# Kernel optimization log

Measured on AMD Instinct MI355X. Metric: run time of the kernel, lower is better.

## Reference

```python
import jax, jax.numpy as jnp
import numpy as np

TOP_K = 2


def setup_inputs() -> dict:
    key = jax.random.key(0)
    k0, k1, k2, k3, k4 = jax.random.split(key, 5)
    B, S, H, I, E = 4, 2048, 1024, 2816, 8
    s_h = 1.0 / np.sqrt(H)
    s_i = 1.0 / np.sqrt(I)
    return {
        "x": jax.random.normal(k0, (B, S, H), jnp.float32),
        # nn.Linear weights are stored as [out_features, in_features]
        "w_router": jax.random.normal(k1, (E, H), jnp.float32) * s_h,   # gate: H -> E
        "w_gate": jax.random.normal(k2, (E, I, H), jnp.float32) * s_h,  # per-expert gate_proj
        "w_up": jax.random.normal(k3, (E, I, H), jnp.float32) * s_h,    # per-expert up_proj
        "w_down": jax.random.normal(k4, (E, H, I), jnp.float32) * s_i,  # per-expert down_proj
    }


def reference(x, w_router, w_gate, w_up, w_down):
    B, S, H = x.shape
    E = w_router.shape[0]
    xf = x.reshape(-1, H)                      # [T, H], T = B*S

    # --- Router: softmax over experts, top-k, renormalize weights ---
    logits = jnp.einsum("th,eh->te", xf, w_router)        # [T, E]
    probs = jax.nn.softmax(logits, axis=-1)
    topw, topi = jax.lax.top_k(probs, TOP_K)              # [T, k]
    topw = topw / jnp.sum(topw, axis=-1, keepdims=True)

    # Per-token combine weight for each expert: sum_k w[t,k] * 1[idx[t,k]==e]
    onehot = (topi[..., None] == jnp.arange(E)).astype(x.dtype)  # [T, k, E]
    combine = jnp.einsum("tk,tke->te", topw, onehot)             # [T, E]

    # --- Experts: SwiGLU MLP per expert on all tokens, masked combine ---
    # (masked-dense in the original == gather-compute mathematically,
    # since silu(0)*0 = 0 and the projections have no bias)
    gate = jax.nn.silu(jnp.einsum("th,eih->eti", xf, w_gate))    # [E, T, I]
    up = jnp.einsum("th,eih->eti", xf, w_up)                     # [E, T, I]
    down = jnp.einsum("eti,ehi->eth", gate * up, w_down)         # [E, T, H]

    out = jnp.einsum("eth,te->th", down, combine)                # [T, H]
    return out.reshape(B, S, H)
```

## Files before the change

### kernel.cpp

```cpp
#include <hip/hip_runtime.h>

#define TT 8192
#define HD 1024
#define ID 2816
#define NE 8
#define NID2 (2*ID)

typedef __attribute__((ext_vector_type(8))) short short8;
typedef __attribute__((ext_vector_type(4))) float f32x4;

#define WS_TOP2I 0
#define WS_TOP2W 65536
#define WS_CNT   131072
#define WS_OFF   131136
#define WS_CUR   131200
#define WS_TMAP  131328
#define WS_SLOTW 196864
#define WS_T2S   262400
#define WS_XB    1048576ULL
#define WS_WGU   (WS_XB  + 16777216ULL)
#define WS_WDB   (WS_WGU + 92274688ULL)
#define WS_ACT   (WS_WDB + 46137344ULL)

__device__ __forceinline__ unsigned int pack_bf2(float lo, float hi) {
  unsigned int ul = __builtin_bit_cast(unsigned int, lo) + 0x8000u;
  unsigned int uh = __builtin_bit_cast(unsigned int, hi) + 0x8000u;
  return (uh & 0xffff0000u) | (ul >> 16);
}

__device__ __forceinline__ unsigned short f2bf(float f) {
  unsigned int u = __builtin_bit_cast(unsigned int, f);
  return (unsigned short)((u + 0x8000u) >> 16);
}

__device__ __forceinline__ void gload16(const void* g, void* l) {
  __builtin_amdgcn_global_load_lds(
      (const __attribute__((address_space(1))) unsigned int*)g,
      (__attribute__((address_space(3))) unsigned int*)l, 16, 0, 0);
}

__global__ __launch_bounds__(256) void router_kernel(
    const float* __restrict__ x, const float* __restrict__ wr,
    int* __restrict__ top2i, float* __restrict__ top2w,
    unsigned short* __restrict__ xb)
{
  int tid  = threadIdx.x;
  int lane = tid & 63;
  int t    = blockIdx.x * 4 + (tid >> 6);

  const float4* xp = (const float4*)(x + (size_t)t * HD + lane * 16);
  float4 xv[4];
  #pragma unroll
  for (int j = 0; j < 4; ++j) xv[j] = xp[j];

  uint4 v0, v1;
  v0.x = pack_bf2(xv[0].x, xv[0].y); v0.y = pack_bf2(xv[0].z, xv[0].w);
  v0.z = pack_bf2(xv[1].x, xv[1].y); v0.w = pack_bf2(xv[1].z, xv[1].w);
  v1.x = pack_bf2(xv[2].x, xv[2].y); v1.y = pack_bf2(xv[2].z, xv[2].w);
  v1.z = pack_bf2(xv[3].x, xv[3].y); v1.w = pack_bf2(xv[3].z, xv[3].w);
  uint4* xrow = (uint4*)(xb + (size_t)t * HD + lane * 16);
  xrow[0] = v0; xrow[1] = v1;

  float acc[NE];
  #pragma unroll
  for (int e = 0; e < NE; ++e) {
    const float4* wp = (const float4*)(wr + (size_t)e * HD + lane * 16);
    float s = 0.f;
    #pragma unroll
    for (int j = 0; j < 4; ++j) {
      float4 w = wp[j];
      s += xv[j].x * w.x + xv[j].y * w.y + xv[j].z * w.z + xv[j].w * w.w;
    }
    acc[e] = s;
  }
  #pragma unroll
  for (int d = 1; d < 64; d <<= 1) {
    #pragma unroll
    for (int e = 0; e < NE; ++e) acc[e] += __shfl_xor(acc[e], d, 64);
  }
  int   i0 = 0; float m0 = acc[0];
  #pragma unroll
  for (int e = 1; e < NE; ++e) if (acc[e] > m0) { m0 = acc[e]; i0 = e; }
  int   i1 = -1; float m1 = -3.4e38f;
  #pragma unroll
  for (int e = 0; e < NE; ++e) if (e != i0 && acc[e] > m1) { m1 = acc[e]; i1 = e; }

  float e1 = __expf(m1 - m0);
  float w0 = 1.f / (1.f + e1);
  float w1 = e1 * w0;

  if (lane == 0) {
    top2i[2 * t] = i0;  top2i[2 * t + 1] = i1;
    top2w[2 * t] = w0;  top2w[2 * t + 1] = w1;
  }
}

__global__ __launch_bounds__(256) void count_scan_kernel(
    const int* __restrict__ top2i,
    int* __restrict__ counts, int* __restrict__ offsets, int* __restrict__ cursors)
{
  __shared__ int s_cnt[NE];
  int tid = threadIdx.x;
  if (tid < NE) s_cnt[tid] = 0;
  __syncthreads();

  int c0=0,c1=0,c2=0,c3=0,c4=0,c5=0,c6=0,c7=0;
  for (int t = tid; t < TT; t += 256) {
    int e0 = top2i[2 * t], e1 = top2i[2 * t + 1];
    c0 += __popcll(__ballot(e0 == 0)) + __popcll(__ballot(e1 == 0));
    c1 += __popcll(__ballot(e0 == 1)) + __popcll(__ballot(e1 == 1));
    c2 += __popcll(__ballot(e0 == 2)) + __popcll(__ballot(e1 == 2));
    c3 += __popcll(__ballot(e0 == 3)) + __popcll(__ballot(e1 == 3));
    c4 += __popcll(__ballot(e0 == 4)) + __popcll(__ballot(e1 == 4));
    c5 += __popcll(__ballot(e0 == 5)) + __popcll(__ballot(e1 == 5));
    c6 += __popcll(__ballot(e0 == 6)) + __popcll(__ballot(e1 == 6));
    c7 += __popcll(__ballot(e0 == 7)) + __popcll(__ballot(e1 == 7));
  }
  if ((tid & 63) == 0) {
    atomicAdd(&s_cnt[0], c0); atomicAdd(&s_cnt[1], c1);
    atomicAdd(&s_cnt[2], c2); atomicAdd(&s_cnt[3], c3);
    atomicAdd(&s_cnt[4], c4); atomicAdd(&s_cnt[5], c5);
    atomicAdd(&s_cnt[6], c6); atomicAdd(&s_cnt[7], c7);
  }
  __syncthreads();
  if (tid == 0) {
    int run = 0;
    #pragma unroll
    for (int e = 0; e < NE; ++e) {
      counts[e] = s_cnt[e]; offsets[e] = run; cursors[e] = run; run += s_cnt[e];
    }
    offsets[NE] = run;
  }
}

__global__ __launch_bounds__(256) void place_kernel(
    const int* __restrict__ top2i, const float* __restrict__ top2w,
    int* __restrict__ cursors,
    int* __restrict__ token_map, float* __restrict__ slot_w, int* __restrict__ tok2slot)
{
  int tid  = threadIdx.x;
  int lane = tid & 63;
  int t    = blockIdx.x * 256 + tid;

  #pragma unroll
  for (int k = 0; k < 2; ++k) {
    int   e = top2i[2 * t + k];
    float w = top2w[2 * t + k];
    #pragma unroll
    for (int ee = 0; ee < NE; ++ee) {
      unsigned long long m = __ballot(e == ee);
      if (e == ee) {
        int leader = __ffsll((long long)m) - 1;
        int pre    = __popcll(m & ((1ull << lane) - 1ull));
        int base   = 0;
        if (lane == leader) base = atomicAdd(&cursors[ee], (int)__popcll(m));
        base = __shfl(base, leader, 64);
        token_map[base + pre] = t;
        slot_w[base + pre]    = w;
        tok2slot[2 * t + k]   = base + pre;
      }
    }
  }
}

__global__ __launch_bounds__(256) void cvt_wgu_kernel(
    const float* __restrict__ wg, const float* __restrict__ wu,
    unsigned short* __restrict__ wgu)
{
  int e   = blockIdx.y;
  int idx = blockIdx.x * 256 + threadIdx.x;
  int col8 = idx & 127;
  int rr   = idx >> 7;
  int blk  = rr >> 8;
  int win  = rr & 255;
  const float* srow = (win < 128)
      ? wg + ((size_t)e * ID + blk * 128 + win) * HD
      : wu + ((size_t)e * ID + blk * 128 + (win - 128)) * HD;
  const float4* p = (const float4*)(srow + col8 * 8);
  float4 a = p[0], b = p[1];
  uint4 v;
  v.x = pack_bf2(a.x, a.y); v.y = pack_bf2(a.z, a.w);
  v.z = pack_bf2(b.x, b.y); v.w = pack_bf2(b.z, b.w);
  *(uint4*)(wgu + ((size_t)e * NID2 + rr) * HD + col8 * 8) = v;
}

__global__ __launch_bounds__(256) void cvt_bf16_kernel(
    const float* __restrict__ in, unsigned short* __restrict__ out, int n8)
{
  int i = blockIdx.x * 256 + threadIdx.x;
  if (i >= n8) return;
  const float4* p = (const float4*)(in + (size_t)i * 8);
  float4 a = p[0], b = p[1];
  uint4 v;
  v.x = pack_bf2(a.x, a.y); v.y = pack_bf2(a.z, a.w);
  v.z = pack_bf2(b.x, b.y); v.w = pack_bf2(b.z, b.w);
  ((uint4*)out)[i] = v;
}


#define VW2() asm volatile("s_waitcnt vmcnt(2)" ::: "memory")
#define VW0() asm volatile("s_waitcnt vmcnt(0)" ::: "memory")
#define LG0() asm volatile("s_waitcnt lgkmcnt(0)" ::: "memory")
#define BAR() __builtin_amdgcn_s_barrier()

#define DBUF(u) (ldsc + (((u) & 1) ? 65536u : 0u) + (unsigned)tid * 16)
#define ISS_B01(u) { size_t k1 = (size_t)((u) * 64); char* db = DBUF(u); \
    gload16(bS[0] + k1, db + 32768); gload16(bS[1] + k1, db + 40960); }
#define ISS_B23(u) { size_t k1 = (size_t)((u) * 64); char* db = DBUF(u); \
    gload16(bS[2] + k1, db + 49152); gload16(bS[3] + k1, db + 57344); }
#define ISS_A02(u) { size_t k1 = (size_t)((u) * 64); char* db = DBUF(u); \
    gload16(aS[0] + k1, db);         gload16(aS[2] + k1, db + 16384); }
#define ISS_A13(u) { size_t k1 = (size_t)((u) * 64); char* db = DBUF(u); \
    gload16(aS[1] + k1, db + 8192);  gload16(aS[3] + k1, db + 24576); }

#define RD_B(KB) \
    _Pragma("unroll") for (int n = 0; n < 4; ++n) \
      bfr[n] = *(const short8*)(sB + (wc * 64 + n * 16 + arow) * 128 + ((KB) ^ rxor));
#define RD_A(MH, KB) \
    _Pragma("unroll") for (int m = 0; m < 4; ++m) \
      af[m] = *(const short8*)(sa + (wr * 128 + (MH) * 64 + m * 16 + arow) * 128 + ((KB) ^ rxor));
#define MF(MB) \
    __builtin_amdgcn_s_setprio(1); \
    _Pragma("unroll") for (int m = 0; m < 4; ++m) \
      _Pragma("unroll") for (int n = 0; n < 4; ++n) \
        acc[(MB) + m][n] = __builtin_amdgcn_mfma_f32_16x16x32_bf16(af[m], bfr[n], acc[(MB) + m][n], 0, 0, 0); \
    __builtin_amdgcn_s_setprio(0);

#define KTILE(t, NT) { \
    const char* sa = ldsc + (((t) & 1) ? 65536u : 0u); \
    const char* sB = sa + 32768; \
    short8 bfr[4], af[4]; \
    int u1 = (t) + 1, u2 = (t) + 2; \
     RD_B(kq) RD_A(0, kq) \
    if (u1 < (NT)) ISS_B23(u1); \
    BAR(); LG0(); MF(0) BAR(); \
     RD_A(1, kq) \
    if (u1 < (NT)) ISS_A02(u1); \
    BAR(); LG0(); MF(4) BAR(); \
     RD_B(64 + kq) RD_A(0, 64 + kq) \
    if (u1 < (NT)) ISS_A13(u1); \
    BAR(); LG0(); MF(0) BAR(); \
     RD_A(1, 64 + kq) \
    if (u2 < (NT)) { ISS_B01(u2); VW2(); } \
    else if (u1 < (NT)) { VW0(); } \
    BAR(); LG0(); MF(4) BAR(); }

#define KLOOP(NT) { \
    ISS_B01(0); ISS_B23(0); ISS_A02(0); ISS_A13(0); \
    ISS_B01(1); \
    VW2(); BAR(); \
    for (int t = 0; t < (NT); ++t) KTILE(t, (NT)); }

#define XCD_DECODE(NX, NY) \
  int nwg  = (NX) * (NY) * NE; \
  int flat = blockIdx.x + (NX) * (blockIdx.y + (NY) * blockIdx.z); \
  int qq   = nwg >> 3; \
  int wg   = (flat & 7) * qq + (flat >> 3); \
  int bx   = wg % (NX); \
  int rem  = wg / (NX); \
  int y    = rem % (NY); \
  int e    = rem / (NY);

__global__ __launch_bounds__(512) void gemm1_fast(
    const unsigned short* __restrict__ xb, const unsigned short* __restrict__ wgu,
    const int* __restrict__ counts, const int* __restrict__ offsets,
    const int* __restrict__ token_map, unsigned short* __restrict__ act)
{
  extern __shared__ char smem[];
  char* ldsc = smem;

  XCD_DECODE(8, 22)
  int cnt = counts[e];
  int off = offsets[e];

  int tid  = threadIdx.x;
  int lane = tid & 63;
  int w    = tid >> 6;
  int wr   = w >> 2;
  int wc   = w & 3;

  int srow0 = tid >> 3;
  int colE  = (((tid & 7) ^ ((tid >> 3) & 7)) << 3);
  int rxor  = (lane & 7) << 4;
  int arow  = lane & 15;
  int kq    = (lane >> 4) << 4;
  int prow  = (lane >> 4) << 2;

  for (int t0 = bx * 256; t0 < cnt; t0 += 2048) {
    const unsigned short* aS[4];
    const unsigned short* bS[4];
    #pragma unroll
    for (int j = 0; j < 4; ++j) {
      int row  = srow0 + 64 * j;
      int tr   = t0 + row;
      int slot = off + (tr < cnt ? tr : cnt - 1);
      aS[j] = xb  + (size_t)token_map[slot] * HD + colE;
      bS[j] = wgu + ((size_t)e * NID2 + (size_t)y * 256 + row) * HD + colE;
    }

    f32x4 zf = {0.f, 0.f, 0.f, 0.f};
    f32x4 acc[8][4];
    #pragma unroll
    for (int m = 0; m < 8; ++m)
      #pragma unroll
      for (int n = 0; n < 4; ++n) acc[m][n] = zf;

    KLOOP(HD / 64);

    __syncthreads();
    float* xch = (float*)smem;
    if (wc >= 2) {
      float* base = xch + (size_t)((wr * 2 + (wc - 2)) * 8192);
      #pragma unroll
      for (int m = 0; m < 8; ++m)
        #pragma unroll
        for (int n = 0; n < 4; ++n)
          #pragma unroll
          for (int r = 0; r < 4; ++r)
            base[(m * 16 + prow + r) * 64 + n * 16 + arow] = acc[m][n][r];
    }
    __syncthreads();
    if (wc < 2) {
      const float* base = xch + (size_t)((wr * 2 + wc) * 8192);
      int i0 = y * 128 + wc * 64;
      #pragma unroll
      for (int m = 0; m < 8; ++m) {
        #pragma unroll
        for (int r = 0; r < 4; ++r) {
          int row = wr * 128 + m * 16 + prow + r;
          int tr2 = t0 + row;
          if (tr2 >= cnt) continue;
          size_t ob = (size_t)(off + tr2) * ID + i0 + arow;
          #pragma unroll
          for (int n = 0; n < 4; ++n) {
            float g = acc[m][n][r];
            float u = base[(m * 16 + prow + r) * 64 + n * 16 + arow];
            float h = g * u / (1.f + __expf(-g));
            act[ob + n * 16] = f2bf(h);
          }
        }
      }
    }
    __syncthreads();
  }
}

__global__ __launch_bounds__(512) void gemm2_fast(
    const unsigned short* __restrict__ act, const unsigned short* __restrict__ wdb,
    const int* __restrict__ counts, const int* __restrict__ offsets,
    float* __restrict__ down)
{
  extern __shared__ char smem[];
  char* ldsc = smem;

  XCD_DECODE(8, 4)
  int cnt = counts[e];
  int off = offsets[e];

  int tid  = threadIdx.x;
  int lane = tid & 63;
  int w    = tid >> 6;
  int wr   = w >> 2;
  int wc   = w & 3;

  int srow0 = tid >> 3;
  int colE  = (((tid & 7) ^ ((tid >> 3) & 7)) << 3);
  int rxor  = (lane & 7) << 4;
  int arow  = lane & 15;
  int kq    = (lane >> 4) << 4;
  int prow  = (lane >> 4) << 2;

  for (int t0 = bx * 256; t0 < cnt; t0 += 2048) {
    const unsigned short* aS[4];
    const unsigned short* bS[4];
    #pragma unroll
    for (int j = 0; j < 4; ++j) {
      int row  = srow0 + 64 * j;
      int tr   = t0 + row;
      int slot = off + (tr < cnt ? tr : cnt - 1);
      aS[j] = act + (size_t)slot * ID + colE;
      bS[j] = wdb + ((size_t)e * HD + (size_t)y * 256 + row) * ID + colE;
    }

    f32x4 zf = {0.f, 0.f, 0.f, 0.f};
    f32x4 acc[8][4];
    #pragma unroll
    for (int m = 0; m < 8; ++m)
      #pragma unroll
      for (int n = 0; n < 4; ++n) acc[m][n] = zf;

    KLOOP(ID / 64);

    #pragma unroll
    for (int m = 0; m < 8; ++m) {
      #pragma unroll
      for (int r = 0; r < 4; ++r) {
        int row = wr * 128 + m * 16 + prow + r;
        int tr2 = t0 + row;
        if (tr2 >= cnt) continue;
        float* ob = down + (size_t)(off + tr2) * HD + (size_t)y * 256 + wc * 64 + arow;
        #pragma unroll
        for (int n = 0; n < 4; ++n)
          ob[n * 16] = acc[m][n][r];
      }
    }
    __syncthreads();
  }
}

__global__ __launch_bounds__(256) void combine_kernel(
    const float* __restrict__ down, const float* __restrict__ slot_w,
    const int* __restrict__ tok2slot, float* __restrict__ out)
{
  int t   = blockIdx.x;
  int tid = threadIdx.x;
  int s0  = tok2slot[2 * t], s1 = tok2slot[2 * t + 1];
  float w0 = slot_w[s0], w1 = slot_w[s1];
  const float4* d0 = (const float4*)(down + (size_t)s0 * HD) + tid;
  const float4* d1 = (const float4*)(down + (size_t)s1 * HD) + tid;
  float4 a = *d0, b = *d1;
  float4 o;
  o.x = w0 * a.x + w1 * b.x;  o.y = w0 * a.y + w1 * b.y;
  o.z = w0 * a.z + w1 * b.z;  o.w = w0 * a.w + w1 * b.w;
  ((float4*)(out + (size_t)t * HD))[tid] = o;
}

extern "C" void kernel_launch(void* const* d_in, const int* in_sizes, int n_in,
                              void* d_out, int out_size, void* d_ws, size_t ws_size,
                              hipStream_t stream) {
  const float* x        = (const float*)d_in[0];
  const float* w_router = (const float*)d_in[1];
  const float* w_gate   = (const float*)d_in[2];
  const float* w_up     = (const float*)d_in[3];
  const float* w_down   = (const float*)d_in[4];

  char* ws = (char*)d_ws;
  int*   top2i    = (int*)(ws + WS_TOP2I);
  float* top2w    = (float*)(ws + WS_TOP2W);
  int*   counts   = (int*)(ws + WS_CNT);
  int*   offsets  = (int*)(ws + WS_OFF);
  int*   cursors  = (int*)(ws + WS_CUR);
  int*   tmap     = (int*)(ws + WS_TMAP);
  float* slotw    = (float*)(ws + WS_SLOTW);
  int*   tok2slot = (int*)(ws + WS_T2S);
  unsigned short* xb  = (unsigned short*)(ws + WS_XB);
  unsigned short* wgu = (unsigned short*)(ws + WS_WGU);
  unsigned short* wdb = (unsigned short*)(ws + WS_WDB);
  unsigned short* act = (unsigned short*)(ws + WS_ACT);
  float*          down = (float*)(ws + WS_WGU);

  hipFuncSetAttribute((const void*)gemm1_fast,
                      hipFuncAttributeMaxDynamicSharedMemorySize, 131072);
  hipFuncSetAttribute((const void*)gemm2_fast,
                      hipFuncAttributeMaxDynamicSharedMemorySize, 131072);

  router_kernel<<<TT / 4, 256, 0, stream>>>(x, w_router, top2i, top2w, xb);
  count_scan_kernel<<<1, 256, 0, stream>>>(top2i, counts, offsets, cursors);
  place_kernel<<<TT / 256, 256, 0, stream>>>(top2i, top2w, cursors, tmap, slotw, tok2slot);
  cvt_wgu_kernel<<<dim3(2816, NE), 256, 0, stream>>>(w_gate, w_up, wgu);
  cvt_bf16_kernel<<<11264, 256, 0, stream>>>(w_down, wdb, NE * HD * ID / 8);

  gemm1_fast<<<dim3(8, 22, NE), 512, 131072, stream>>>(xb, wgu, counts, offsets, tmap, act);
  gemm2_fast<<<dim3(8, 4, NE), 512, 131072, stream>>>(act, wdb, counts, offsets, down);
  combine_kernel<<<TT, 256, 0, stream>>>(down, slotw, tok2slot, (float*)d_out);
}
```

Baseline: 594.1 us.

## Restructure GEMM K-loop pipeline with fewer barriers and inline-asm LDS reads

Rewrites the K-tile loop of the expert GEMM. Per-tile barriers drop from eight to two: each tile now waits on vmcnt(1), syncs once, and then issues the next tile's global-to-LDS loads in between the LDS reads and MFMA groups. The last tile is peeled so the main loop has no branches. LDS fragment reads now go through explicit ds_read_b128 inline asm with a sched_barrier after lgkmcnt waits, to control how instructions are ordered. The cost is a shorter prefetch distance, since the B01 half is no longer issued two tiles ahead, so global-load latency may be less well hidden.

```diff
diff --git a/kernel.cpp b/kernel.cpp
--- a/kernel.cpp
+++ b/kernel.cpp
@@ -37,6 +37,13 @@
   __builtin_amdgcn_global_load_lds(
       (const __attribute__((address_space(1))) unsigned int*)g,
       (__attribute__((address_space(3))) unsigned int*)l, 16, 0, 0);
+}
+
+__device__ __forceinline__ short8 dsr(const void* p) {
+  short8 d;
+  unsigned a = (unsigned)(size_t)(__attribute__((address_space(3))) const char*)p;
+  asm volatile("ds_read_b128 %0, %1" : "=v"(d) : "v"(a));
+  return d;
 }
 
 __global__ __launch_bounds__(256) void router_kernel(
@@ -198,9 +205,10 @@
 }
 
 
-#define VW2() asm volatile("s_waitcnt vmcnt(2)" ::: "memory")
+#define VW1() asm volatile("s_waitcnt vmcnt(1)" ::: "memory")
 #define VW0() asm volatile("s_waitcnt vmcnt(0)" ::: "memory")
-#define LG0() asm volatile("s_waitcnt lgkmcnt(0)" ::: "memory")
+#define LGS() { asm volatile("s_waitcnt lgkmcnt(0)" ::: "memory"); \
+                __builtin_amdgcn_sched_barrier(0); }
 #define BAR() __builtin_amdgcn_s_barrier()
 
 #define DBUF(u) (ldsc + (((u) & 1) ? 65536u : 0u) + (unsigned)tid * 16)
@@ -213,12 +221,11 @@
 #define ISS_A13(u) { size_t k1 = (size_t)((u) * 64); char* db = DBUF(u); \
     gload16(aS[1] + k1, db + 8192);  gload16(aS[3] + k1, db + 24576); }
 
-#define RD_B(KB) \
-    _Pragma("unroll") for (int n = 0; n < 4; ++n) \
-      bfr[n] = *(const short8*)(sB + (wc * 64 + n * 16 + arow) * 128 + ((KB) ^ rxor));
-#define RD_A(MH, KB) \
-    _Pragma("unroll") for (int m = 0; m < 4; ++m) \
-      af[m] = *(const short8*)(sa + (wr * 128 + (MH) * 64 + m * 16 + arow) * 128 + ((KB) ^ rxor));
+#define RDB(KB) { _Pragma("unroll") for (int n = 0; n < 4; ++n) \
+    bfr[n] = dsr(sB + (wc * 64 + n * 16 + arow) * 128 + ((KB) ^ rxor)); }
+#define RDA(MH, KB) { _Pragma("unroll") for (int m = 0; m < 4; ++m) \
+    af[m] = dsr(sa + (wr * 128 + (MH) * 64 + m * 16 + arow) * 128 + ((KB) ^ rxor)); }
+
 #define MF(MB) \
     __builtin_amdgcn_s_setprio(1); \
     _Pragma("unroll") for (int m = 0; m < 4; ++m) \
@@ -226,30 +233,29 @@
         acc[(MB) + m][n] = __builtin_amdgcn_mfma_f32_16x16x32_bf16(af[m], bfr[n], acc[(MB) + m][n], 0, 0, 0); \
     __builtin_amdgcn_s_setprio(0);
 
-#define KTILE(t, NT) { \
+#define KTILE_MAIN(t) { \
     const char* sa = ldsc + (((t) & 1) ? 65536u : 0u); \
     const char* sB = sa + 32768; \
     short8 bfr[4], af[4]; \
-    int u1 = (t) + 1, u2 = (t) + 2; \
-     RD_B(kq) RD_A(0, kq) \
-    if (u1 < (NT)) ISS_B23(u1); \
-    BAR(); LG0(); MF(0) BAR(); \
-     RD_A(1, kq) \
-    if (u1 < (NT)) ISS_A02(u1); \
-    BAR(); LG0(); MF(4) BAR(); \
-     RD_B(64 + kq) RD_A(0, 64 + kq) \
-    if (u1 < (NT)) ISS_A13(u1); \
-    BAR(); LG0(); MF(0) BAR(); \
-     RD_A(1, 64 + kq) \
-    if (u2 < (NT)) { ISS_B01(u2); VW2(); } \
-    else if (u1 < (NT)) { VW0(); } \
-    BAR(); LG0(); MF(4) BAR(); }
+    int u1 = (t) + 1; \
+    VW1(); BAR(); ISS_B01(u1); RDB(kq) RDA(0, kq) LGS(); MF(0) \
+    VW1(); BAR(); ISS_B23(u1); RDA(1, kq) LGS(); MF(4) \
+    ISS_A02(u1); RDB(64 + kq) RDA(0, 64 + kq) LGS(); MF(0) \
+    ISS_A13(u1); RDA(1, 64 + kq) LGS(); MF(4) }
+
+#define KTILE_LAST(t) { \
+    const char* sa = ldsc + (((t) & 1) ? 65536u : 0u); \
+    const char* sB = sa + 32768; \
+    short8 bfr[4], af[4]; \
+    VW1(); BAR(); RDB(kq) RDA(0, kq) LGS(); MF(0) \
+    VW0(); BAR(); RDA(1, kq) LGS(); MF(4) \
+    RDB(64 + kq) RDA(0, 64 + kq) LGS(); MF(0) \
+    RDA(1, 64 + kq) LGS(); MF(4) }
 
 #define KLOOP(NT) { \
     ISS_B01(0); ISS_B23(0); ISS_A02(0); ISS_A13(0); \
-    ISS_B01(1); \
-    VW2(); BAR(); \
-    for (int t = 0; t < (NT); ++t) KTILE(t, (NT)); }
+    for (int t = 0; t < (NT) - 1; ++t) KTILE_MAIN(t); \
+    KTILE_LAST((NT) - 1); }
 
 #define XCD_DECODE(NX, NY) \
   int nwg  = (NX) * (NY) * NE; \
```

Measured after the change: 604.2 us. About the same (+1.7%).
